# Performance work log

Measured on AMD Instinct MI355X. Metric: run time of the kernel, lower is better.

## Reference

```python
import jax, jax.numpy as jnp
import numpy as np

MAGBIAS = 0.01
INV_SQRT2 = np.float32(1.0 / np.sqrt(2.0))


def _reflect(x, minx, maxx):
    # Half-sample symmetric reflection of indices (static numpy; matches dtcwt reflect()).
    rng = maxx - minx
    mod = np.fmod(x - minx, 2.0 * rng)
    mod = np.where(mod < 0, mod + 2.0 * rng, mod)
    out = np.where(mod >= rng, 2.0 * rng - mod, mod) + minx
    return np.round(out).astype(np.int64)


def _symm_pad(l, m):
    return _reflect(np.arange(-m, l + m, dtype=np.float64), -0.5, l - 0.5)


def _depthwise(X, h, axis, stride):
    # Per-channel 1-D correlation along rows (axis=2) or cols (axis=3), NCHW, like F.conv2d(groups=ch).
    ch = X.shape[1]
    if axis == 2:
        k = h.reshape(1, 1, -1, 1)
        strides = (stride, 1)
    else:
        k = h.reshape(1, 1, 1, -1)
        strides = (1, stride)
    k = jnp.tile(k, (ch, 1, 1, 1)).astype(X.dtype)
    return jax.lax.conv_general_dilated(
        X, k, window_strides=strides, padding='VALID',
        dimension_numbers=('NCHW', 'OIHW', 'NCHW'), feature_group_count=ch)


def colfilter(X, h):
    m = h.shape[0] // 2
    xe = _symm_pad(X.shape[2], m)
    return _depthwise(X[:, :, xe, :], h, axis=2, stride=1)


def rowfilter(X, h):
    m = h.shape[0] // 2
    xe = _symm_pad(X.shape[3], m)
    return _depthwise(X[:, :, :, xe], h, axis=3, stride=1)


def coldfilt(X, ha, hb, highpass):
    # Dual-tree decimated column filtering with a quarter-shift pair; output rows = r // 2.
    b, ch, r, c = X.shape
    m = ha.shape[0]
    xe = _symm_pad(r, m)
    ya = _depthwise(X[:, :, xe[2::2], :], ha, axis=2, stride=2)  # (b,ch,r/4,c)
    yb = _depthwise(X[:, :, xe[3::2], :], hb, axis=2, stride=2)
    first, second = (yb, ya) if highpass else (ya, yb)
    return jnp.stack([first, second], axis=3).reshape(b, ch, r // 2, c)


def rowdfilt(X, ha, hb, highpass):
    b, ch, r, c = X.shape
    m = ha.shape[0]
    xe = _symm_pad(c, m)
    ya = _depthwise(X[:, :, :, xe[2::2]], ha, axis=3, stride=2)
    yb = _depthwise(X[:, :, :, xe[3::2]], hb, axis=3, stride=2)
    first, second = (yb, ya) if highpass else (ya, yb)
    return jnp.stack([first, second], axis=4).reshape(b, ch, r, c // 2)


def q2c(y):
    # Quads -> two complex subbands (real, imag): the DTCWT butterfly combine.
    y = y * INV_SQRT2
    a = y[..., 0::2, 0::2]
    b = y[..., 0::2, 1::2]
    c = y[..., 1::2, 0::2]
    d = y[..., 1::2, 1::2]
    return (a - d, b + c), (a + d, b - c)


def _stack_orients(lh, hl, hh):
    (d15r, d15i), (d165r, d165i) = q2c(lh)
    (d45r, d45i), (d135r, d135i) = q2c(hh)
    (d75r, d75i), (d105r, d105i) = q2c(hl)
    reals = jnp.stack([d15r, d45r, d75r, d105r, d135r, d165r], axis=1)
    imags = jnp.stack([d15i, d45i, d75i, d105i, d135i, d165i], axis=1)
    return reals, imags


def fwd_j1(x, h0, h1):
    # Level-1 DTCWT: undecimated separable biorthogonal filters + q2c.
    lo = rowfilter(x, h0)
    hi = rowfilter(x, h1)
    ll = colfilter(lo, h0)
    lh = colfilter(lo, h1)
    hl = colfilter(hi, h0)
    hh = colfilter(hi, h1)
    reals, imags = _stack_orients(lh, hl, hh)
    return ll, reals, imags


def fwd_j2plus(x, h0a, h1a, h0b, h1b):
    # Level-2 DTCWT: decimated quarter-shift filter pairs + q2c.
    lo = rowdfilt(x, h0b, h0a, False)
    hi = rowdfilt(x, h1b, h1a, True)
    ll = coldfilt(lo, h0b, h0a, False)
    lh = coldfilt(lo, h1b, h1a, True)
    hl = coldfilt(hi, h0b, h0a, False)
    hh = coldfilt(hi, h1b, h1a, True)
    reals, imags = _stack_orients(lh, hl, hh)
    return ll, reals, imags


def _smooth_mag(re, im, bias):
    return jnp.sqrt(re * re + im * im + bias * bias) - bias


def _avgpool2(x):
    b, ch, r, c = x.shape
    return x.reshape(b, ch, r // 2, 2, c // 2, 2).mean(axis=(3, 5))


def _scat_forward(x, h0o, h1o, h0a, h0b, h1a, h1b):
    b, ch, r, c = x.shape  # r, c multiples of 8 (input already padded)
    # First order, scale j=1
    ll, re, im = fwd_j1(x, h0o, h1o)
    s1_j1 = _smooth_mag(re, im, MAGBIAS)                      # (b,6,ch,r/2,c/2)
    # First order, scale j=2 (on the running lowpass)
    ll, re, im = fwd_j2plus(ll, h0a, h1a, h0b, h1b)           # ll: (b,ch,r/2,c/2)
    s1_j2 = _smooth_mag(re, im, MAGBIAS)                      # (b,6,ch,r/4,c/4)
    # Second order: one more octave on the first-order magnitudes
    p = s1_j1.reshape(b, 6 * ch, r // 2, c // 2)
    p, re, im = fwd_j1(p, h0o, h1o)
    s2 = _smooth_mag(re, im, MAGBIAS).reshape(b, 36, ch, r // 4, c // 4)
    s0 = _avgpool2(ll)[:, None]                               # (b,1,ch,r/4,c/4)
    s1_j1 = _avgpool2(p).reshape(b, 6, ch, r // 4, c // 4)
    Z = jnp.concatenate([s0, s1_j1, s1_j2, s2], axis=1)       # (b,49,ch,r/4,c/4)
    return Z.reshape(b, 49 * ch, r // 4, c // 4)


def setup_inputs():
    key = jax.random.key(0)
    ks = jax.random.split(key, 5)
    x = jax.random.normal(ks[0], (32, 3, 512, 512), dtype=jnp.float32)
    h0o = jax.random.normal(ks[1], (5,), dtype=jnp.float32) * 0.3
    h1o = jax.random.normal(ks[2], (7,), dtype=jnp.float32) * 0.3
    h0a = jax.random.normal(ks[3], (10,), dtype=jnp.float32) * 0.3
    h1a = jax.random.normal(ks[4], (10,), dtype=jnp.float32) * 0.3
    h0b = h0a[::-1]  # quarter-shift pair: time-reverse of the tree-a filter
    h1b = h1a[::-1]
    return {"x": x, "h0o": h0o, "h1o": h1o, "h0a": h0a, "h0b": h0b,
            "h1a": h1a, "h1b": h1b}


def reference(x, h0o, h1o, h0a, h0b, h1a, h1b):
    return _scat_forward(x, h0o, h1o, h0a, h0b, h1a, h1b)
```

## Files before the change

kernel.cpp:

```cpp
#include <hip/hip_runtime.h>

#define IS2 0.70710678118654752440f

__device__ __forceinline__ int refl(int i, int n) {
    if (i < 0) i = -1 - i;
    if (i >= n) i = 2 * n - 1 - i;
    return i;
}

__device__ __forceinline__ float smag(float re, float im) {
    return sqrtf(re * re + im * im + 1.0e-4f) - 0.01f;
}

__device__ __forceinline__ void mag2(const float y[2][2], float* mA, float* mB) {
    float a = y[0][0] * IS2, b = y[0][1] * IS2;
    float c = y[1][0] * IS2, d = y[1][1] * IS2;
    *mA = smag(a - d, b + c);
    *mB = smag(a + d, b - c);
}

template <int MODE>
__global__ __launch_bounds__(256, 4)
void fwd_j1_kernel(const float* __restrict__ in,
                   const float* __restrict__ h0,
                   const float* __restrict__ h1,
                   float* __restrict__ ll_out,
                   float* __restrict__ mag_out,
                   int CH, int N)
{
    const int img = blockIdx.z;
    const int b   = img / CH;
    const int chn = img % CH;
    const int ty0 = blockIdx.y * 64;
    const int tx0 = blockIdx.x * 64;
    const int tid = threadIdx.x;

    __shared__ float sx[70 * 72];
    __shared__ float slo[70 * 64];

    float f0[5], f1[7];
#pragma unroll
    for (int t = 0; t < 5; ++t) f0[t] = h0[t];
#pragma unroll
    for (int t = 0; t < 7; ++t) f1[t] = h1[t];

    const float* src = in + (size_t)img * N * N;

    for (int e = tid; e < 70 * 70; e += 256) {
        int rr = e / 70, cc = e % 70;
        int gr = refl(ty0 - 3 + rr, N);
        int gc = refl(tx0 - 3 + cc, N);
        sx[rr * 72 + cc] = src[(size_t)gr * N + gc];
    }
    __syncthreads();

    float vlo[18], vhi[18];
#pragma unroll
    for (int k = 0; k < 18; ++k) {
        int e = tid + k * 256;
        if (e < 70 * 64) {
            int rr = e >> 6, j = e & 63;
            const float* row = &sx[rr * 72];
            float lo = 0.f, hi = 0.f;
#pragma unroll
            for (int t = 0; t < 5; ++t) lo += row[j + 1 + t] * f0[t];
#pragma unroll
            for (int t = 0; t < 7; ++t) hi += row[j + t] * f1[t];
            vlo[k] = lo; vhi[k] = hi;
        }
    }
    __syncthreads();
#pragma unroll
    for (int k = 0; k < 18; ++k) {
        int e = tid + k * 256;
        if (e < 70 * 64) {
            slo[e] = vlo[k];
            sx[e]  = vhi[k];
        }
    }
    __syncthreads();

    const int Nh = N >> 1;
    for (int e = tid; e < 32 * 32; e += 256) {
        int qi = e >> 5, qj = e & 31;
        float ll4[2][2], lh4[2][2], hl4[2][2], hh4[2][2];
#pragma unroll
        for (int di = 0; di < 2; ++di) {
#pragma unroll
            for (int dj = 0; dj < 2; ++dj) {
                int i = 2 * qi + di, j = 2 * qj + dj;
                float vll = 0.f, vlh = 0.f, vhl = 0.f, vhh = 0.f;
#pragma unroll
                for (int t = 0; t < 5; ++t) {
                    vll += slo[(i + 1 + t) * 64 + j] * f0[t];
                    vhl += sx [(i + 1 + t) * 64 + j] * f0[t];
                }
#pragma unroll
                for (int t = 0; t < 7; ++t) {
                    vlh += slo[(i + t) * 64 + j] * f1[t];
                    vhh += sx [(i + t) * 64 + j] * f1[t];
                }
                ll4[di][dj] = vll; lh4[di][dj] = vlh;
                hl4[di][dj] = vhl; hh4[di][dj] = vhh;
            }
        }

        const int qy = (ty0 >> 1) + qi;
        const int qx = (tx0 >> 1) + qj;

        float m[6];
        mag2(lh4, &m[0], &m[5]);
        mag2(hh4, &m[1], &m[4]);
        mag2(hl4, &m[2], &m[3]);

        if (MODE == 0) {
            float* lptr = ll_out + (size_t)img * N * N;
            *(float2*)(lptr + (size_t)(ty0 + 2 * qi) * N + tx0 + 2 * qj) =
                make_float2(ll4[0][0], ll4[0][1]);
            *(float2*)(lptr + (size_t)(ty0 + 2 * qi + 1) * N + tx0 + 2 * qj) =
                make_float2(ll4[1][0], ll4[1][1]);
#pragma unroll
            for (int o = 0; o < 6; ++o) {
                mag_out[(((size_t)b * 6 + o) * CH + chn) * (size_t)(Nh * Nh)
                        + (size_t)qy * Nh + qx] = m[o];
            }
        } else {
            const int o1 = chn / 3, c = chn % 3;
            float* Zb = mag_out + (size_t)b * 147 * 16384 + (size_t)qy * 128 + qx;
#pragma unroll
            for (int o2 = 0; o2 < 6; ++o2) {
                Zb[(size_t)((13 + o2 * 6 + o1) * 3 + c) * 16384] = m[o2];
            }
            float pll = 0.25f * (ll4[0][0] + ll4[0][1] + ll4[1][0] + ll4[1][1]);
            Zb[(size_t)((1 + o1) * 3 + c) * 16384] = pll;
        }
    }
}

__global__ __launch_bounds__(256, 4)
void fwd_j2_kernel(const float* __restrict__ ll,
                   const float* __restrict__ h0a, const float* __restrict__ h0b,
                   const float* __restrict__ h1a, const float* __restrict__ h1b,
                   float* __restrict__ Z)
{
    const int img = blockIdx.z;
    const int b = img / 3, c = img % 3;
    const int r0 = blockIdx.y * 32;
    const int c0 = blockIdx.x * 32;
    const int tid = threadIdx.x;

    __shared__ float sx[80 * 84];
    float* const sloP = sx;
    float* const shiP = sx + 2688;

    float fa0[10], fb0[10], fa1[10], fb1[10];
#pragma unroll
    for (int t = 0; t < 10; ++t) {
        fa0[t] = h0a[t]; fb0[t] = h0b[t];
        fa1[t] = h1a[t]; fb1[t] = h1b[t];
    }

    const float* src = ll + (size_t)img * 512 * 512;

    for (int e = tid; e < 80 * 80; e += 256) {
        int rr = e / 80, cc = e % 80;
        int gr = refl(2 * r0 - 8 + rr, 512);
        int gc = refl(2 * c0 - 8 + cc, 512);
        sx[rr * 84 + cc] = src[(size_t)gr * 512 + gc];
    }
    __syncthreads();

    const int jj  = tid & 31;
    const int odd = jj & 1;
    const int base = 2 * (jj & ~1);
    float hlo[10], hhi[10];
#pragma unroll
    for (int t = 0; t < 10; ++t) {
        hlo[t] = odd ? fa0[t] : fb0[t];
        hhi[t] = odd ? fb1[t] : fa1[t];
    }
    const int offlo = base + odd;
    const int offhi = base + 1 - odd;
    float rlo[10], rhi[10];
#pragma unroll
    for (int k = 0; k < 10; ++k) {
        int rr = (tid >> 5) + 8 * k;
        const float* row = &sx[rr * 84];
        float lo = 0.f, hi = 0.f;
#pragma unroll
        for (int t = 0; t < 10; ++t) {
            lo += row[offlo + 2 * t] * hlo[t];
            hi += row[offhi + 2 * t] * hhi[t];
        }
        rlo[k] = lo; rhi[k] = hi;
    }
    __syncthreads();
#pragma unroll
    for (int k = 0; k < 10; ++k) {
        int rr = (tid >> 5) + 8 * k;
        sloP[rr * 33 + jj] = rlo[k];
        shiP[rr * 33 + jj] = rhi[k];
    }
    __syncthreads();

    const int qi = tid >> 4, qj = tid & 15;
    float ll2[2][2], lh4[2][2], hl4[2][2], hh4[2][2];
#pragma unroll
    for (int dj = 0; dj < 2; ++dj) {
        const int col = 2 * qj + dj;
        const int rb  = 4 * qi;
        float vll0 = 0.f, vll1 = 0.f, vlh0 = 0.f, vlh1 = 0.f;
        float vhl0 = 0.f, vhl1 = 0.f, vhh0 = 0.f, vhh1 = 0.f;
#pragma unroll
        for (int t = 0; t < 10; ++t) {
            float e0 = sloP[(rb + 2 * t) * 33 + col];
            float e1 = sloP[(rb + 2 * t + 1) * 33 + col];
            float g0 = shiP[(rb + 2 * t) * 33 + col];
            float g1 = shiP[(rb + 2 * t + 1) * 33 + col];
            vll0 += e0 * fb0[t];
            vll1 += e1 * fa0[t];
            vlh0 += e1 * fa1[t];
            vlh1 += e0 * fb1[t];
            vhl0 += g0 * fb0[t];
            vhl1 += g1 * fa0[t];
            vhh0 += g1 * fa1[t];
            vhh1 += g0 * fb1[t];
        }
        ll2[0][dj] = vll0; ll2[1][dj] = vll1;
        lh4[0][dj] = vlh0; lh4[1][dj] = vlh1;
        hl4[0][dj] = vhl0; hl4[1][dj] = vhl1;
        hh4[0][dj] = vhh0; hh4[1][dj] = vhh1;
    }

    const int qy = (r0 >> 1) + qi;
    const int qx = (c0 >> 1) + qj;
    float* Zb = Z + (size_t)b * 147 * 16384 + (size_t)qy * 128 + qx;

    Zb[(size_t)c * 16384] =
        0.25f * (ll2[0][0] + ll2[0][1] + ll2[1][0] + ll2[1][1]);

    float m[6];
    mag2(lh4, &m[0], &m[5]);
    mag2(hh4, &m[1], &m[4]);
    mag2(hl4, &m[2], &m[3]);
#pragma unroll
    for (int o = 0; o < 6; ++o) {
        Zb[(size_t)((7 + o) * 3 + c) * 16384] = m[o];
    }
}

extern "C" void kernel_launch(void* const* d_in, const int* in_sizes, int n_in,
                              void* d_out, int out_size, void* d_ws, size_t ws_size,
                              hipStream_t stream)
{
    const float* x   = (const float*)d_in[0];
    const float* h0o = (const float*)d_in[1];
    const float* h1o = (const float*)d_in[2];
    const float* h0a = (const float*)d_in[3];
    const float* h0b = (const float*)d_in[4];
    const float* h1a = (const float*)d_in[5];
    const float* h1b = (const float*)d_in[6];
    float* Z = (float*)d_out;

    float* ws_ll = (float*)d_ws;
    float* ws_p  = ws_ll + (size_t)32 * 3 * 512 * 512;

    dim3 blk(256);
    fwd_j1_kernel<0><<<dim3(8, 8, 96), blk, 0, stream>>>(x, h0o, h1o, ws_ll, ws_p, 3, 512);
    fwd_j2_kernel<<<dim3(8, 8, 96), blk, 0, stream>>>(ws_ll, h0a, h0b, h1a, h1b, Z);
    fwd_j1_kernel<1><<<dim3(4, 4, 576), blk, 0, stream>>>(ws_p, h0o, h1o, nullptr, Z, 18, 256);
}
```

Before: 632.9 us.

## Register-block row and column filters in fwd_j1 with shuffle-based quad combine

The horizontal pass of fwd_j1 now has each thread compute 4 adjacent outputs from a 12-float window read with vectorized float4 LDS loads, and stores them with float4 writes. The vertical pass assigns each thread one column and a 16-row strip, caching 22 column values in registers so shared-memory reads are reused across output rows. Lane pairs exchange values through __shfl_xor to form the complex quad magnitudes, so each lane writes one magnitude plane instead of one thread writing all six. This cuts LDS traffic and redundant filter loads, but raises register pressure and changes the global write pattern.

Result: no change. 630.3 us (-0.4%).

```diff
diff --git a/kernel.cpp b/kernel.cpp
--- a/kernel.cpp
+++ b/kernel.cpp
@@ -10,13 +10,6 @@
 
 __device__ __forceinline__ float smag(float re, float im) {
     return sqrtf(re * re + im * im + 1.0e-4f) - 0.01f;
-}
-
-__device__ __forceinline__ void mag2(const float y[2][2], float* mA, float* mB) {
-    float a = y[0][0] * IS2, b = y[0][1] * IS2;
-    float c = y[1][0] * IS2, d = y[1][1] * IS2;
-    *mA = smag(a - d, b + c);
-    *mB = smag(a + d, b - c);
 }
 
 template <int MODE>
@@ -35,8 +28,9 @@
     const int tx0 = blockIdx.x * 64;
     const int tid = threadIdx.x;
 
-    __shared__ float sx[70 * 72];
-    __shared__ float slo[70 * 64];
+    __shared__ __align__(16) float sx[70 * 72];
+    __shared__ __align__(16) float slo[70 * 64];
+    float* const shi = sx;
 
     float f0[5], f1[7];
 #pragma unroll
@@ -54,85 +48,119 @@
     }
     __syncthreads();
 
-    float vlo[18], vhi[18];
-#pragma unroll
-    for (int k = 0; k < 18; ++k) {
+    float rlo[5][4], rhi[5][4];
+#pragma unroll
+    for (int k = 0; k < 5; ++k) {
         int e = tid + k * 256;
-        if (e < 70 * 64) {
-            int rr = e >> 6, j = e & 63;
-            const float* row = &sx[rr * 72];
-            float lo = 0.f, hi = 0.f;
-#pragma unroll
-            for (int t = 0; t < 5; ++t) lo += row[j + 1 + t] * f0[t];
-#pragma unroll
-            for (int t = 0; t < 7; ++t) hi += row[j + t] * f1[t];
-            vlo[k] = lo; vhi[k] = hi;
-        }
-    }
-    __syncthreads();
-#pragma unroll
-    for (int k = 0; k < 18; ++k) {
+        if (e < 1120) {
+            int rr = e >> 4, g = e & 15;
+            const float4* w4 = (const float4*)&sx[rr * 72 + 4 * g];
+            float4 wa = w4[0], wb = w4[1], wc = w4[2];
+            float win[12] = {wa.x, wa.y, wa.z, wa.w,
+                             wb.x, wb.y, wb.z, wb.w,
+                             wc.x, wc.y, wc.z, wc.w};
+#pragma unroll
+            for (int u = 0; u < 4; ++u) {
+                float lo = 0.f, hi = 0.f;
+#pragma unroll
+                for (int t = 0; t < 5; ++t) lo += win[u + 1 + t] * f0[t];
+#pragma unroll
+                for (int t = 0; t < 7; ++t) hi += win[u + t] * f1[t];
+                rlo[k][u] = lo; rhi[k][u] = hi;
+            }
+        }
+    }
+    __syncthreads();
+#pragma unroll
+    for (int k = 0; k < 5; ++k) {
         int e = tid + k * 256;
-        if (e < 70 * 64) {
-            slo[e] = vlo[k];
-            sx[e]  = vhi[k];
-        }
-    }
-    __syncthreads();
-
-    const int Nh = N >> 1;
-    for (int e = tid; e < 32 * 32; e += 256) {
-        int qi = e >> 5, qj = e & 31;
-        float ll4[2][2], lh4[2][2], hl4[2][2], hh4[2][2];
-#pragma unroll
-        for (int di = 0; di < 2; ++di) {
-#pragma unroll
-            for (int dj = 0; dj < 2; ++dj) {
-                int i = 2 * qi + di, j = 2 * qj + dj;
-                float vll = 0.f, vlh = 0.f, vhl = 0.f, vhh = 0.f;
-#pragma unroll
-                for (int t = 0; t < 5; ++t) {
-                    vll += slo[(i + 1 + t) * 64 + j] * f0[t];
-                    vhl += sx [(i + 1 + t) * 64 + j] * f0[t];
-                }
-#pragma unroll
-                for (int t = 0; t < 7; ++t) {
-                    vlh += slo[(i + t) * 64 + j] * f1[t];
-                    vhh += sx [(i + t) * 64 + j] * f1[t];
-                }
-                ll4[di][dj] = vll; lh4[di][dj] = vlh;
-                hl4[di][dj] = vhl; hh4[di][dj] = vhh;
+        if (e < 1120) {
+            int rr = e >> 4, g = e & 15;
+            *(float4*)&slo[rr * 64 + 4 * g] =
+                make_float4(rlo[k][0], rlo[k][1], rlo[k][2], rlo[k][3]);
+            *(float4*)&shi[rr * 64 + 4 * g] =
+                make_float4(rhi[k][0], rhi[k][1], rhi[k][2], rhi[k][3]);
+        }
+    }
+    __syncthreads();
+
+    const int j     = tid & 63;
+    const int rg    = tid >> 6;
+    const int rbase = rg * 16;
+
+    float clo[22], chi[22];
+#pragma unroll
+    for (int t = 0; t < 22; ++t) {
+        clo[t] = slo[(rbase + t) * 64 + j];
+        chi[t] = shi[(rbase + t) * 64 + j];
+    }
+
+    const int Nh  = N >> 1;
+    const int par = j & 1;
+    const int qx  = (tx0 >> 1) + (j >> 1);
+    const int qy0 = (ty0 >> 1) + rg * 8;
+    const int oLH = par ? 5 : 0;
+    const int oHH = par ? 4 : 1;
+    const int oHL = par ? 3 : 2;
+
+    float* lcol = nullptr;
+    float* pLH = nullptr; float* pHH = nullptr; float* pHL = nullptr;
+    float* zBase = nullptr;
+    size_t zLH = 0, zHH = 0, zHL = 0, zPL = 0;
+    if (MODE == 0) {
+        lcol = ll_out + (size_t)img * N * N + (size_t)(ty0 + rbase) * N + tx0 + j;
+        const size_t planeSz = (size_t)Nh * Nh;
+        const size_t qoff = (size_t)qy0 * Nh + qx;
+        pLH = mag_out + ((size_t)(b * 6 + oLH) * CH + chn) * planeSz + qoff;
+        pHH = mag_out + ((size_t)(b * 6 + oHH) * CH + chn) * planeSz + qoff;
+        pHL = mag_out + ((size_t)(b * 6 + oHL) * CH + chn) * planeSz + qoff;
+    } else {
+        const int o1 = chn / 3, c3 = chn % 3;
+        zBase = mag_out + (size_t)b * 147 * 16384 + (size_t)qy0 * 128 + qx;
+        zLH = (size_t)((13 + oLH * 6 + o1) * 3 + c3) * 16384;
+        zHH = (size_t)((13 + oHH * 6 + o1) * 3 + c3) * 16384;
+        zHL = (size_t)((13 + oHL * 6 + o1) * 3 + c3) * 16384;
+        zPL = (size_t)((1 + o1) * 3 + c3) * 16384;
+    }
+
+#pragma unroll
+    for (int ii = 0; ii < 8; ++ii) {
+        const int i0 = 2 * ii, i1 = 2 * ii + 1;
+        float ll0 = 0.f, ll1 = 0.f, lh0 = 0.f, lh1 = 0.f;
+        float hl0 = 0.f, hl1 = 0.f, hh0 = 0.f, hh1 = 0.f;
+#pragma unroll
+        for (int t = 0; t < 5; ++t) {
+            ll0 += clo[i0 + 1 + t] * f0[t]; ll1 += clo[i1 + 1 + t] * f0[t];
+            hl0 += chi[i0 + 1 + t] * f0[t]; hl1 += chi[i1 + 1 + t] * f0[t];
+        }
+#pragma unroll
+        for (int t = 0; t < 7; ++t) {
+            lh0 += clo[i0 + t] * f1[t]; lh1 += clo[i1 + t] * f1[t];
+            hh0 += chi[i0 + t] * f1[t]; hh1 += chi[i1 + t] * f1[t];
+        }
+
+        float lhT = __shfl_xor(lh0, 1), lhB = __shfl_xor(lh1, 1);
+        float hhT = __shfl_xor(hh0, 1), hhB = __shfl_xor(hh1, 1);
+        float hlT = __shfl_xor(hl0, 1), hlB = __shfl_xor(hl1, 1);
+        float mLH = smag(IS2 * (lh0 - lhB), IS2 * (lhT + lh1));
+        float mHH = smag(IS2 * (hh0 - hhB), IS2 * (hhT + hh1));
+        float mHL = smag(IS2 * (hl0 - hlB), IS2 * (hlT + hl1));
+
+        if (MODE == 0) {
+            lcol[(size_t)i0 * N] = ll0;
+            lcol[(size_t)i1 * N] = ll1;
+            pLH[(size_t)ii * Nh] = mLH;
+            pHH[(size_t)ii * Nh] = mHH;
+            pHL[(size_t)ii * Nh] = mHL;
+        } else {
+            float* zr = zBase + (size_t)ii * 128;
+            zr[zLH] = mLH;
+            zr[zHH] = mHH;
+            zr[zHL] = mHL;
+            float llT = __shfl_xor(ll0, 1), llB = __shfl_xor(ll1, 1);
+            if (par == 0) {
+                zr[zPL] = 0.25f * (ll0 + ll1 + llT + llB);
             }
-        }
-
-        const int qy = (ty0 >> 1) + qi;
-        const int qx = (tx0 >> 1) + qj;
-
-        float m[6];
-        mag2(lh4, &m[0], &m[5]);
-        mag2(hh4, &m[1], &m[4]);
-        mag2(hl4, &m[2], &m[3]);
-
-        if (MODE == 0) {
-            float* lptr = ll_out + (size_t)img * N * N;
-            *(float2*)(lptr + (size_t)(ty0 + 2 * qi) * N + tx0 + 2 * qj) =
-                make_float2(ll4[0][0], ll4[0][1]);
-            *(float2*)(lptr + (size_t)(ty0 + 2 * qi + 1) * N + tx0 + 2 * qj) =
-                make_float2(ll4[1][0], ll4[1][1]);
-#pragma unroll
-            for (int o = 0; o < 6; ++o) {
-                mag_out[(((size_t)b * 6 + o) * CH + chn) * (size_t)(Nh * Nh)
-                        + (size_t)qy * Nh + qx] = m[o];
-            }
-        } else {
-            const int o1 = chn / 3, c = chn % 3;
-            float* Zb = mag_out + (size_t)b * 147 * 16384 + (size_t)qy * 128 + qx;
-#pragma unroll
-            for (int o2 = 0; o2 < 6; ++o2) {
-                Zb[(size_t)((13 + o2 * 6 + o1) * 3 + c) * 16384] = m[o2];
-            }
-            float pll = 0.25f * (ll4[0][0] + ll4[0][1] + ll4[1][0] + ll4[1][1]);
-            Zb[(size_t)((1 + o1) * 3 + c) * 16384] = pll;
         }
     }
 }
@@ -239,13 +267,19 @@
     Zb[(size_t)c * 16384] =
         0.25f * (ll2[0][0] + ll2[0][1] + ll2[1][0] + ll2[1][1]);
 
-    float m[6];
-    mag2(lh4, &m[0], &m[5]);
-    mag2(hh4, &m[1], &m[4]);
-    mag2(hl4, &m[2], &m[3]);
-#pragma unroll
-    for (int o = 0; o < 6; ++o) {
-        Zb[(size_t)((7 + o) * 3 + c) * 16384] = m[o];
+    {
+        float a, bq, cq, d;
+        float m[6];
+        a = lh4[0][0] * IS2; bq = lh4[0][1] * IS2; cq = lh4[1][0] * IS2; d = lh4[1][1] * IS2;
+        m[0] = smag(a - d, bq + cq); m[5] = smag(a + d, bq - cq);
+        a = hh4[0][0] * IS2; bq = hh4[0][1] * IS2; cq = hh4[1][0] * IS2; d = hh4[1][1] * IS2;
+        m[1] = smag(a - d, bq + cq); m[4] = smag(a + d, bq - cq);
+        a = hl4[0][0] * IS2; bq = hl4[0][1] * IS2; cq = hl4[1][0] * IS2; d = hl4[1][1] * IS2;
+        m[2] = smag(a - d, bq + cq); m[3] = smag(a + d, bq - cq);
+#pragma unroll
+        for (int o = 0; o < 6; ++o) {
+            Zb[(size_t)((7 + o) * 3 + c) * 16384] = m[o];
+        }
     }
 }
 
```
